# Kernel tuning notes

Hardware: AMD Instinct MI355X
Metric: run time of the kernel (lower is better)

The kernel has to match this reference:

```python
import jax, jax.numpy as jnp
import numpy as np

EPS = 1e-5

def conv1x1(x, w):
    # x: [B,C,T,D,H,W], w: [O,C] -> [B,O,T,D,H,W]
    return jnp.einsum('oc,bctdhw->botdhw', w, x)

def conv4d_3(x, w):
    # 3x3x3x3 4D conv, padding=1, stride=1, decomposed as 3 shifted 3D convs.
    # x: [B,C,T,D,H,W], w: [O,C,3,3,3,3]
    B, C, T, D, H, W = x.shape
    O = w.shape[0]
    xp = jnp.pad(x, ((0, 0), (0, 0), (1, 1), (1, 1), (1, 1), (1, 1)))
    out = None
    for k in range(3):  # small fixed loop over first kernel dim
        xk = xp[:, :, k:k + T]                      # [B,C,T,D+2,H+2,W+2]
        xk = xk.transpose(0, 2, 1, 3, 4, 5).reshape(B * T, C, D + 2, H + 2, W + 2)
        ok = jax.lax.conv_general_dilated(
            xk, w[:, :, k], window_strides=(1, 1, 1), padding='VALID',
            dimension_numbers=('NCDHW', 'OIDHW', 'NCDHW'))  # [B*T,O,D,H,W]
        out = ok if out is None else out + ok
    return out.reshape(B, T, O, D, H, W).transpose(0, 2, 1, 3, 4, 5)

def bn4d(x, g, b):
    # BatchNorm over (B, T, D, H, W) per channel (training-mode batch stats).
    axes = (0, 2, 3, 4, 5)
    m = jnp.mean(x, axis=axes, keepdims=True)
    v = jnp.mean(jnp.square(x - m), axis=axes, keepdims=True)
    sh = (1, -1, 1, 1, 1, 1)
    return (x - m) * jax.lax.rsqrt(v + EPS) * g.reshape(sh) + b.reshape(sh)

def setup_inputs() -> dict:
    key = jax.random.key(0)
    ks = jax.random.split(key, 4)
    B, C, T, D, H, W = 2, 256, 8, 16, 16, 16
    planes = 64
    return {
        'x': jax.random.normal(ks[0], (B, C, T, D, H, W), jnp.float32),
        'w1': jax.random.normal(ks[1], (planes, C), jnp.float32) * 0.05,
        'g1': jnp.ones((planes,), jnp.float32),
        'b1': jnp.zeros((planes,), jnp.float32),
        'w2': jax.random.normal(ks[2], (planes, planes, 3, 3, 3, 3), jnp.float32) * 0.05,
        'g2': jnp.ones((planes,), jnp.float32),
        'b2': jnp.zeros((planes,), jnp.float32),
        'w3': jax.random.normal(ks[3], (4 * planes, planes), jnp.float32) * 0.05,
        'g3': jnp.ones((4 * planes,), jnp.float32),
        'b3': jnp.zeros((4 * planes,), jnp.float32),
    }

def reference(x, w1, g1, b1, w2, g2, b2, w3, g3, b3):
    out = jax.nn.relu(bn4d(conv1x1(x, w1), g1, b1))
    out = jax.nn.relu(bn4d(conv4d_3(out, w2), g2, b2))
    out = bn4d(conv1x1(out, w3), g3, b3)
    return jax.nn.relu(out + x)
```

## Files before the change

kernel.cpp:

```cpp
#include <hip/hip_runtime.h>

#define S_TOT 32768

typedef unsigned short ushortT;
typedef __attribute__((ext_vector_type(8))) short short8;
typedef __attribute__((ext_vector_type(4))) float floatx4;

__device__ __forceinline__ ushortT f2bf(float f) {
    unsigned u = __float_as_uint(f);
    u = (u + 0x7fffu + ((u >> 16) & 1u)) >> 16;
    return (ushortT)u;
}
__device__ __forceinline__ float bf2f(ushortT h) {
    return __uint_as_float(((unsigned)h) << 16);
}
__device__ __forceinline__ uint32_t nrm2(uint32_t u, float a, float bs) {
    float lo = fmaxf(fmaf(a, bf2f((ushortT)(u & 0xffffu)), bs), 0.f);
    float hi = fmaxf(fmaf(a, bf2f((ushortT)(u >> 16)), bs), 0.f);
    return (uint32_t)f2bf(lo) | ((uint32_t)f2bf(hi) << 16);
}

#define NSTRIPE 8
#define STRIDE_ST 768

__global__ __launch_bounds__(256) void k_prep_w(const float* __restrict__ w1,
                                                const float* __restrict__ w2,
                                                const float* __restrict__ w3,
                                                ushortT* __restrict__ wb1,
                                                ushortT* __restrict__ wb2,
                                                ushortT* __restrict__ wb3,
                                                float* __restrict__ stats) {
    int idx = blockIdx.x * 256 + threadIdx.x;
    if (idx < 16384) {
        int e = idx;
        int j = e & 7, o = (e >> 3) & 63, q = (e >> 9) & 3, cc = e >> 11;
        int c = cc * 32 + q * 8 + j;
        wb1[e] = f2bf(w1[o * 256 + c]);
    } else if (idx < 16384 + 331776) {
        int e = idx - 16384;
        int j = e & 7, o = (e >> 3) & 63, cb = (e >> 9) & 7, tap = e >> 12;
        int c = cb * 8 + j;
        wb2[e] = f2bf(w2[((size_t)o * 64 + c) * 81 + tap]);
    } else if (idx < 16384 + 331776 + 16384) {
        int e = idx - 348160;
        int j = e & 7, o = (e >> 3) & 255, g = e >> 11;
        int ks = g >> 2, q = g & 3;
        int c = ks * 32 + q * 8 + j;
        wb3[e] = f2bf(w3[o * 64 + c]);
    } else if (idx < 364544 + NSTRIPE * STRIDE_ST) {
        stats[idx - 364544] = 0.f;
    }
}

__global__ __launch_bounds__(256) void k_coef(const float* __restrict__ stats,
                                              int off, int nch,
                                              const float* __restrict__ g,
                                              const float* __restrict__ bb,
                                              float* __restrict__ coef) {
    int c = threadIdx.x;
    if (c >= nch) return;
    float s = 0.f, qv = 0.f;
#pragma unroll
    for (int p = 0; p < NSTRIPE; ++p) {
        s  += stats[p * STRIDE_ST + off + c];
        qv += stats[p * STRIDE_ST + off + nch + c];
    }
    const float inv_n = 1.f / 65536.f;
    float mu = s * inv_n, var = qv * inv_n - mu * mu;
    float a  = g[c] * rsqrtf(var + 1e-5f);
    coef[2 * c]     = a;
    coef[2 * c + 1] = bb[c] - mu * a;
}

__global__ __launch_bounds__(256) void k_conv1_mfma(const float* __restrict__ x,
                                                    const ushortT* __restrict__ wb1,
                                                    ushortT* __restrict__ y1bf,
                                                    float* __restrict__ stats) {
    __shared__ __align__(16) ushortT xb[128 * 40];

    int tid = threadIdx.x;
    int blk = blockIdx.x;
    int b  = blk >> 8;
    int n0 = (blk & 255) * 128;

    int lane = tid & 63;
    int wv   = tid >> 6;
    int m    = lane & 15;
    int q    = lane >> 4;

    int c_loc = tid & 31;
    int ng    = tid >> 5;

    floatx4 acc[8];
#pragma unroll
    for (int i = 0; i < 8; ++i) acc[i] = (floatx4){0.f, 0.f, 0.f, 0.f};

    for (int cc = 0; cc < 8; ++cc) {
        short8 afr = *(const short8*)(wb1 + (((cc * 4 + q) * 64) + wv * 16 + m) * 8);

        __syncthreads();
        {
            int c = cc * 32 + c_loc;
            const float* xp = x + ((size_t)(b * 256 + c)) * S_TOT + n0 + ng * 16;
#pragma unroll
            for (int k = 0; k < 4; ++k) {
                float4 v = *(const float4*)(xp + k * 4);
                int nb = ng * 16 + k * 4;
                xb[(nb + 0) * 40 + c_loc] = f2bf(v.x);
                xb[(nb + 1) * 40 + c_loc] = f2bf(v.y);
                xb[(nb + 2) * 40 + c_loc] = f2bf(v.z);
                xb[(nb + 3) * 40 + c_loc] = f2bf(v.w);
            }
        }
        __syncthreads();

#pragma unroll
        for (int pt = 0; pt < 8; ++pt) {
            short8 bfr = *(const short8*)(xb + (pt * 16 + m) * 40 + q * 8);
            acc[pt] = __builtin_amdgcn_mfma_f32_16x16x32_bf16(afr, bfr, acc[pt], 0, 0, 0);
        }
    }

#pragma unroll
    for (int pt = 0; pt < 8; ++pt) {
#pragma unroll
        for (int r = 0; r < 4; ++r) {
            int o = wv * 16 + q * 4 + r;
            y1bf[((size_t)(b * 64 + o)) * S_TOT + n0 + pt * 16 + m] = f2bf(acc[pt][r]);
        }
    }

    float ssum[4] = {0.f, 0.f, 0.f, 0.f}, ssq[4] = {0.f, 0.f, 0.f, 0.f};
#pragma unroll
    for (int pt = 0; pt < 8; ++pt)
#pragma unroll
        for (int r = 0; r < 4; ++r) {
            float v = acc[pt][r];
            ssum[r] += v;
            ssq[r]  += v * v;
        }
#pragma unroll
    for (int off = 1; off < 16; off <<= 1)
#pragma unroll
        for (int r = 0; r < 4; ++r) {
            ssum[r] += __shfl_xor(ssum[r], off);
            ssq[r]  += __shfl_xor(ssq[r], off);
        }
    if (m == 0) {
        float* st = stats + (blk & (NSTRIPE - 1)) * STRIDE_ST;
#pragma unroll
        for (int r = 0; r < 4; ++r) {
            int o = wv * 16 + q * 4 + r;
            atomicAdd(st + o, ssum[r]);
            atomicAdd(st + 64 + o, ssq[r]);
        }
    }
}

__global__ __launch_bounds__(256, 2) void k_conv2_mfma(
        const ushortT* __restrict__ y1bf,
        const ushortT* __restrict__ wb2,
        const float* __restrict__ coef1,
        float* __restrict__ stats,
        ushortT* __restrict__ y2bf) {
    __shared__ __align__(16) ushortT xs[180 * 64];
    __shared__ float st2[128];

    int tid = threadIdx.x;
    int blk = blockIdx.x;
    int b  = blk >> 8;
    int t  = (blk >> 5) & 7;
    int d  = (blk >> 1) & 15;
    int h0 = (blk & 1) * 8;

    int lane = tid & 63;
    int wv   = tid >> 6;
    int m    = lane & 15;
    int q    = lane >> 4;
    int wp   = wv & 1;
    int wo   = wv >> 1;

    int c2      = tid & 31;
    int prbase  = tid >> 5;

    if (tid < 128) st2[tid] = 0.f;

    int c0 = 2 * c2, c1v = c0 + 1;
    float2 cA = *(const float2*)(coef1 + 2 * c0);
    float2 cB = *(const float2*)(coef1 + 2 * c1v);
    float a0 = cA.x, bb0 = cA.y, a1 = cB.x, bb1 = cB.y;

    floatx4 acc[2][4];
#pragma unroll
    for (int i = 0; i < 2; ++i)
#pragma unroll
        for (int j = 0; j < 4; ++j) acc[i][j] = (floatx4){0.f, 0.f, 0.f, 0.f};

    const size_t cstride = 32768;
    uint32_t* xsd = (uint32_t*)xs;

    for (int ktd = 0; ktd < 9; ++ktd) {
        int kt = ktd / 3, kd = ktd - kt * 3;
        int tt = t + kt - 1;
        int dd = d + kd - 1;
        bool pv = (tt >= 0 && tt < 8 && dd >= 0 && dd < 16);
        if (!pv) continue;

        short8 afr[9][2][2];
#pragma unroll
        for (int khw = 0; khw < 9; ++khw) {
            int tap = ktd * 9 + khw;
#pragma unroll
            for (int ks = 0; ks < 2; ++ks)
#pragma unroll
                for (int ot = 0; ot < 2; ++ot) {
                    afr[khw][ks][ot] = *(const short8*)(wb2 +
                        (((size_t)(tap * 8 + ks * 4 + q)) * 64 + wo * 32 + ot * 16 + m) * 8);
                }
        }

        __syncthreads();

        for (int pr = prbase; pr < 10; pr += 8) {
            int hin = h0 + pr - 1;
            uint32_t pack[18];
            if (hin >= 0 && hin < 16) {
                const ushortT* p0 = y1bf +
                    (((size_t)(b * 64 + c0) * 8 + tt) * 16 + dd) * 256 + hin * 16;
                const ushortT* p1 = p0 + cstride;
                uint4 r0 = *(const uint4*)p0;
                uint4 r1 = *(const uint4*)(p0 + 8);
                uint4 s0v = *(const uint4*)p1;
                uint4 s1v = *(const uint4*)(p1 + 8);
                uint32_t ra[8] = {r0.x, r0.y, r0.z, r0.w, r1.x, r1.y, r1.z, r1.w};
                uint32_t sa[8] = {s0v.x, s0v.y, s0v.z, s0v.w, s1v.x, s1v.y, s1v.z, s1v.w};
#pragma unroll
                for (int k = 0; k < 8; ++k) {
                    ra[k] = nrm2(ra[k], a0, bb0);
                    sa[k] = nrm2(sa[k], a1, bb1);
                }
                pack[0] = 0; pack[17] = 0;
#pragma unroll
                for (int k = 0; k < 8; ++k) {
                    pack[1 + 2 * k] = (ra[k] & 0xffffu) | (sa[k] << 16);
                    pack[2 + 2 * k] = (ra[k] >> 16) | (sa[k] & 0xffff0000u);
                }
            } else {
#pragma unroll
                for (int k = 0; k < 18; ++k) pack[k] = 0;
            }
            int pb = pr * 18;
#pragma unroll
            for (int k = 0; k < 18; ++k) {
                int ppos = pb + k;
                xsd[ppos * 32 + ((((c2 >> 2) ^ (ppos & 7)) << 2) | (c2 & 3))] = pack[k];
            }
        }
        __syncthreads();

#pragma unroll
        for (int kh = 0; kh < 3; ++kh) {
#pragma unroll
            for (int kw = 0; kw < 3; ++kw) {
                int khw = kh * 3 + kw;
#pragma unroll
                for (int nt = 0; nt < 4; ++nt) {
                    int ppos = (wp * 4 + nt + kh) * 18 + m + kw;
                    int sw = (ppos & 7);
                    const ushortT* row = xs + ppos * 64;
                    short8 b0 = *(const short8*)(row + (((0 * 4 + q) ^ sw) << 3));
                    short8 b1f = *(const short8*)(row + (((1 * 4 + q) ^ sw) << 3));
                    acc[0][nt] = __builtin_amdgcn_mfma_f32_16x16x32_bf16(
                        afr[khw][0][0], b0, acc[0][nt], 0, 0, 0);
                    acc[1][nt] = __builtin_amdgcn_mfma_f32_16x16x32_bf16(
                        afr[khw][0][1], b0, acc[1][nt], 0, 0, 0);
                    acc[0][nt] = __builtin_amdgcn_mfma_f32_16x16x32_bf16(
                        afr[khw][1][0], b1f, acc[0][nt], 0, 0, 0);
                    acc[1][nt] = __builtin_amdgcn_mfma_f32_16x16x32_bf16(
                        afr[khw][1][1], b1f, acc[1][nt], 0, 0, 0);
                }
            }
        }
    }

#pragma unroll
    for (int ot = 0; ot < 2; ++ot) {
#pragma unroll
        for (int nt = 0; nt < 4; ++nt) {
#pragma unroll
            for (int r = 0; r < 4; ++r) {
                int o  = wo * 32 + ot * 16 + q * 4 + r;
                int hh = h0 + wp * 4 + nt;
                y2bf[(((size_t)(b * 64 + o) * 8 + t) * 16 + d) * 256 + hh * 16 + m] =
                    f2bf(acc[ot][nt][r]);
            }
        }
    }

    float ss[2][4], sqv[2][4];
#pragma unroll
    for (int ot = 0; ot < 2; ++ot)
#pragma unroll
        for (int r = 0; r < 4; ++r) {
            float s = 0.f, qv = 0.f;
#pragma unroll
            for (int nt = 0; nt < 4; ++nt) {
                float v = acc[ot][nt][r];
                s += v; qv += v * v;
            }
            ss[ot][r] = s; sqv[ot][r] = qv;
        }
#pragma unroll
    for (int off = 1; off < 16; off <<= 1)
#pragma unroll
        for (int ot = 0; ot < 2; ++ot)
#pragma unroll
            for (int r = 0; r < 4; ++r) {
                ss[ot][r]  += __shfl_xor(ss[ot][r], off);
                sqv[ot][r] += __shfl_xor(sqv[ot][r], off);
            }
    if (m == 0) {
#pragma unroll
        for (int ot = 0; ot < 2; ++ot)
#pragma unroll
            for (int r = 0; r < 4; ++r) {
                int o = wo * 32 + ot * 16 + q * 4 + r;
                atomicAdd(&st2[o], ss[ot][r]);
                atomicAdd(&st2[64 + o], sqv[ot][r]);
            }
    }
    __syncthreads();
    if (tid < 128)
        atomicAdd(stats + (blk & (NSTRIPE - 1)) * STRIDE_ST + 128 + tid, st2[tid]);
}

__global__ __launch_bounds__(256) void k_conv3_mfma(const ushortT* __restrict__ y2bf,
                                                    const ushortT* __restrict__ wb3,
                                                    const float* __restrict__ coef2,
                                                    float* __restrict__ stats,
                                                    float* __restrict__ y3) {
    __shared__ __align__(16) ushortT yb[64 * 72];

    int tid = threadIdx.x;
    int blk = blockIdx.x;
    int b  = blk >> 9;
    int n0 = (blk & 511) * 64;

    int lane = tid & 63;
    int wv   = tid >> 6;
    int m    = lane & 15;
    int q    = lane >> 4;

    for (int idx = tid; idx < 512; idx += 256) {
        int c = idx >> 3, k = idx & 7;
        float2 cc2 = *(const float2*)(coef2 + 2 * c);
        float a = cc2.x, bs = cc2.y;
        uint4 v = *(const uint4*)(y2bf + ((size_t)(b * 64 + c)) * S_TOT + n0 + k * 8);
        uint32_t va[4] = {v.x, v.y, v.z, v.w};
#pragma unroll
        for (int p = 0; p < 4; ++p) {
            float lo = fmaxf(fmaf(a, bf2f((ushortT)(va[p] & 0xffffu)), bs), 0.f);
            float hi = fmaxf(fmaf(a, bf2f((ushortT)(va[p] >> 16)), bs), 0.f);
            yb[(k * 8 + 2 * p)     * 72 + c] = f2bf(lo);
            yb[(k * 8 + 2 * p + 1) * 72 + c] = f2bf(hi);
        }
    }
    __syncthreads();

    floatx4 acc[4][4];
#pragma unroll
    for (int i = 0; i < 4; ++i)
#pragma unroll
        for (int j = 0; j < 4; ++j) acc[i][j] = (floatx4){0.f, 0.f, 0.f, 0.f};

#pragma unroll
    for (int ks = 0; ks < 2; ++ks) {
        short8 afr[4];
#pragma unroll
        for (int ot = 0; ot < 4; ++ot)
            afr[ot] = *(const short8*)(wb3 +
                (((ks * 4 + q) * 256) + wv * 64 + ot * 16 + m) * 8);
#pragma unroll
        for (int pt = 0; pt < 4; ++pt) {
            short8 bfr = *(const short8*)(yb + (pt * 16 + m) * 72 + ks * 32 + q * 8);
#pragma unroll
            for (int ot = 0; ot < 4; ++ot)
                acc[ot][pt] = __builtin_amdgcn_mfma_f32_16x16x32_bf16(
                    afr[ot], bfr, acc[ot][pt], 0, 0, 0);
        }
    }

#pragma unroll
    for (int ot = 0; ot < 4; ++ot) {
#pragma unroll
        for (int pt = 0; pt < 4; ++pt) {
#pragma unroll
            for (int r = 0; r < 4; ++r) {
                int o = wv * 64 + ot * 16 + q * 4 + r;
                y3[((size_t)(b * 256 + o)) * S_TOT + n0 + pt * 16 + m] = acc[ot][pt][r];
            }
        }
    }

    float ssum[4][4], ssq[4][4];
#pragma unroll
    for (int ot = 0; ot < 4; ++ot)
#pragma unroll
        for (int r = 0; r < 4; ++r) {
            float s = 0.f, qv = 0.f;
#pragma unroll
            for (int pt = 0; pt < 4; ++pt) {
                float v = acc[ot][pt][r];
                s += v; qv += v * v;
            }
            ssum[ot][r] = s; ssq[ot][r] = qv;
        }
#pragma unroll
    for (int off = 1; off < 16; off <<= 1)
#pragma unroll
        for (int ot = 0; ot < 4; ++ot)
#pragma unroll
            for (int r = 0; r < 4; ++r) {
                ssum[ot][r] += __shfl_xor(ssum[ot][r], off);
                ssq[ot][r]  += __shfl_xor(ssq[ot][r], off);
            }
    if (m == 0) {
        float* st = stats + (blk & (NSTRIPE - 1)) * STRIDE_ST;
#pragma unroll
        for (int ot = 0; ot < 4; ++ot)
#pragma unroll
            for (int r = 0; r < 4; ++r) {
                int o = wv * 64 + ot * 16 + q * 4 + r;
                atomicAdd(st + 256 + o, ssum[ot][r]);
                atomicAdd(st + 512 + o, ssq[ot][r]);
            }
    }
}

__global__ __launch_bounds__(256) void k_final(const float* __restrict__ x,
                                               const float* __restrict__ stats,
                                               const float* __restrict__ g,
                                               const float* __restrict__ bb,
                                               float* __restrict__ out) {
    size_t i = ((size_t)blockIdx.x * 256 + threadIdx.x) * 4;
    int o = (int)((blockIdx.x >> 5) & 255);
    float s = 0.f, qv = 0.f;
#pragma unroll
    for (int p = 0; p < NSTRIPE; ++p) {
        s  += stats[p * STRIDE_ST + 256 + o];
        qv += stats[p * STRIDE_ST + 512 + o];
    }
    const float n = 65536.f;
    float mean = s / n;
    float var  = qv / n - mean * mean;
    float a  = g[o] * rsqrtf(var + 1e-5f);
    float bs = bb[o] - mean * a;
    float4 y  = *(float4*)(out + i);
    float4 xv = *(const float4*)(x + i);
    float4 r;
    r.x = fmaxf(a * y.x + bs + xv.x, 0.f);
    r.y = fmaxf(a * y.y + bs + xv.y, 0.f);
    r.z = fmaxf(a * y.z + bs + xv.z, 0.f);
    r.w = fmaxf(a * y.w + bs + xv.w, 0.f);
    *(float4*)(out + i) = r;
}

extern "C" void kernel_launch(void* const* d_in, const int* in_sizes, int n_in,
                              void* d_out, int out_size, void* d_ws, size_t ws_size,
                              hipStream_t stream) {
    const float* x  = (const float*)d_in[0];
    const float* w1 = (const float*)d_in[1];
    const float* g1 = (const float*)d_in[2];
    const float* b1 = (const float*)d_in[3];
    const float* w2 = (const float*)d_in[4];
    const float* g2 = (const float*)d_in[5];
    const float* b2 = (const float*)d_in[6];
    const float* w3 = (const float*)d_in[7];
    const float* g3 = (const float*)d_in[8];
    const float* b3 = (const float*)d_in[9];

    char* ws = (char*)d_ws;
    ushortT* y1bf = (ushortT*)(ws);
    ushortT* y2bf = (ushortT*)(ws + 8388608);
    ushortT* wb1  = (ushortT*)(ws + 16777216);
    ushortT* wb2  = (ushortT*)(ws + 16809984);
    ushortT* wb3  = (ushortT*)(ws + 17473536);
    float*   stats = (float*)(ws + 17506304);
    float*   coef1 = (float*)(ws + 17530880);
    float*   coef2 = (float*)(ws + 17531392);
    float* y3 = (float*)d_out;

    k_prep_w     <<<1448,  256, 0, stream>>>(w1, w2, w3, wb1, wb2, wb3, stats);
    k_conv1_mfma <<<512,   256, 0, stream>>>(x, wb1, y1bf, stats);
    k_coef       <<<1,     256, 0, stream>>>(stats, 0, 64, g1, b1, coef1);
    k_conv2_mfma <<<512,   256, 0, stream>>>(y1bf, wb2, coef1, stats, y2bf);
    k_coef       <<<1,     256, 0, stream>>>(stats, 128, 64, g2, b2, coef2);
    k_conv3_mfma <<<1024,  256, 0, stream>>>(y2bf, wb3, coef2, stats, y3);
    k_final      <<<16384, 256, 0, stream>>>(x, stats, g3, b3, y3);
}
```

Measured before the change: 268.5 us.

## Pre-normalize conv1 output in separate pass and halve conv2 spatial tile

Adds a separate elementwise kernel that applies BN1 scale/shift and ReLU to the conv1 output once, writing a normalized bf16 copy. The conv2 kernel then loads that copy directly instead of re-normalizing every halo row for each of the 9 (t,d) taps. Conv2 now covers 4 h-rows per block instead of 8, which doubles the grid, shrinks the shared tile, and raises the occupancy hint to 4. In exchange there is an extra launch, an extra 8 MB read and write to a new workspace buffer, and a larger halo overhead (6 loaded rows per 4 output rows instead of 10 per 8).

```diff
diff --git a/kernel.cpp b/kernel.cpp
--- a/kernel.cpp
+++ b/kernel.cpp
@@ -72,6 +72,21 @@
     coef[2 * c + 1] = bb[c] - mu * a;
 }
 
+__global__ __launch_bounds__(256) void k_prep(const ushortT* __restrict__ yin,
+                                              const float* __restrict__ coef,
+                                              ushortT* __restrict__ yout) {
+    size_t i = ((size_t)blockIdx.x * 256 + threadIdx.x) * 8;
+    int c = (int)((i >> 15) & 63);
+    float2 cf = *(const float2*)(coef + 2 * c);
+    uint4 v = *(const uint4*)(yin + i);
+    uint4 r;
+    r.x = nrm2(v.x, cf.x, cf.y);
+    r.y = nrm2(v.y, cf.x, cf.y);
+    r.z = nrm2(v.z, cf.x, cf.y);
+    r.w = nrm2(v.w, cf.x, cf.y);
+    *(uint4*)(yout + i) = r;
+}
+
 __global__ __launch_bounds__(256) void k_conv1_mfma(const float* __restrict__ x,
                                                     const ushortT* __restrict__ wb1,
                                                     ushortT* __restrict__ y1bf,
@@ -157,21 +172,20 @@
     }
 }
 
-__global__ __launch_bounds__(256, 2) void k_conv2_mfma(
-        const ushortT* __restrict__ y1bf,
+__global__ __launch_bounds__(256, 4) void k_conv2_mfma(
+        const ushortT* __restrict__ y1n,
         const ushortT* __restrict__ wb2,
-        const float* __restrict__ coef1,
         float* __restrict__ stats,
         ushortT* __restrict__ y2bf) {
-    __shared__ __align__(16) ushortT xs[180 * 64];
+    __shared__ __align__(16) ushortT xs[108 * 64];
     __shared__ float st2[128];
 
     int tid = threadIdx.x;
     int blk = blockIdx.x;
-    int b  = blk >> 8;
-    int t  = (blk >> 5) & 7;
-    int d  = (blk >> 1) & 15;
-    int h0 = (blk & 1) * 8;
+    int b  = blk >> 9;
+    int t  = (blk >> 6) & 7;
+    int d  = (blk >> 2) & 15;
+    int h0 = (blk & 3) * 4;
 
     int lane = tid & 63;
     int wv   = tid >> 6;
@@ -185,16 +199,11 @@
 
     if (tid < 128) st2[tid] = 0.f;
 
-    int c0 = 2 * c2, c1v = c0 + 1;
-    float2 cA = *(const float2*)(coef1 + 2 * c0);
-    float2 cB = *(const float2*)(coef1 + 2 * c1v);
-    float a0 = cA.x, bb0 = cA.y, a1 = cB.x, bb1 = cB.y;
-
-    floatx4 acc[2][4];
+    floatx4 acc[2][2];
 #pragma unroll
     for (int i = 0; i < 2; ++i)
 #pragma unroll
-        for (int j = 0; j < 4; ++j) acc[i][j] = (floatx4){0.f, 0.f, 0.f, 0.f};
+        for (int j = 0; j < 2; ++j) acc[i][j] = (floatx4){0.f, 0.f, 0.f, 0.f};
 
     const size_t cstride = 32768;
     uint32_t* xsd = (uint32_t*)xs;
@@ -221,12 +230,12 @@
 
         __syncthreads();
 
-        for (int pr = prbase; pr < 10; pr += 8) {
-            int hin = h0 + pr - 1;
+        if (prbase < 6) {
+            int hin = h0 + prbase - 1;
             uint32_t pack[18];
             if (hin >= 0 && hin < 16) {
-                const ushortT* p0 = y1bf +
-                    (((size_t)(b * 64 + c0) * 8 + tt) * 16 + dd) * 256 + hin * 16;
+                const ushortT* p0 = y1n +
+                    (((size_t)(b * 64 + 2 * c2) * 8 + tt) * 16 + dd) * 256 + hin * 16;
                 const ushortT* p1 = p0 + cstride;
                 uint4 r0 = *(const uint4*)p0;
                 uint4 r1 = *(const uint4*)(p0 + 8);
@@ -234,11 +243,6 @@
                 uint4 s1v = *(const uint4*)(p1 + 8);
                 uint32_t ra[8] = {r0.x, r0.y, r0.z, r0.w, r1.x, r1.y, r1.z, r1.w};
                 uint32_t sa[8] = {s0v.x, s0v.y, s0v.z, s0v.w, s1v.x, s1v.y, s1v.z, s1v.w};
-#pragma unroll
-                for (int k = 0; k < 8; ++k) {
-                    ra[k] = nrm2(ra[k], a0, bb0);
-                    sa[k] = nrm2(sa[k], a1, bb1);
-                }
                 pack[0] = 0; pack[17] = 0;
 #pragma unroll
                 for (int k = 0; k < 8; ++k) {
@@ -249,7 +253,7 @@
 #pragma unroll
                 for (int k = 0; k < 18; ++k) pack[k] = 0;
             }
-            int pb = pr * 18;
+            int pb = prbase * 18;
 #pragma unroll
             for (int k = 0; k < 18; ++k) {
                 int ppos = pb + k;
@@ -264,11 +268,11 @@
             for (int kw = 0; kw < 3; ++kw) {
                 int khw = kh * 3 + kw;
 #pragma unroll
-                for (int nt = 0; nt < 4; ++nt) {
-                    int ppos = (wp * 4 + nt + kh) * 18 + m + kw;
+                for (int nt = 0; nt < 2; ++nt) {
+                    int ppos = (wp * 2 + nt + kh) * 18 + m + kw;
                     int sw = (ppos & 7);
                     const ushortT* row = xs + ppos * 64;
-                    short8 b0 = *(const short8*)(row + (((0 * 4 + q) ^ sw) << 3));
+                    short8 b0  = *(const short8*)(row + (((0 * 4 + q) ^ sw) << 3));
                     short8 b1f = *(const short8*)(row + (((1 * 4 + q) ^ sw) << 3));
                     acc[0][nt] = __builtin_amdgcn_mfma_f32_16x16x32_bf16(
                         afr[khw][0][0], b0, acc[0][nt], 0, 0, 0);
@@ -286,11 +290,11 @@
 #pragma unroll
     for (int ot = 0; ot < 2; ++ot) {
 #pragma unroll
-        for (int nt = 0; nt < 4; ++nt) {
+        for (int nt = 0; nt < 2; ++nt) {
 #pragma unroll
             for (int r = 0; r < 4; ++r) {
                 int o  = wo * 32 + ot * 16 + q * 4 + r;
-                int hh = h0 + wp * 4 + nt;
+                int hh = h0 + wp * 2 + nt;
                 y2bf[(((size_t)(b * 64 + o) * 8 + t) * 16 + d) * 256 + hh * 16 + m] =
                     f2bf(acc[ot][nt][r]);
             }
@@ -304,7 +308,7 @@
         for (int r = 0; r < 4; ++r) {
             float s = 0.f, qv = 0.f;
 #pragma unroll
-            for (int nt = 0; nt < 4; ++nt) {
+            for (int nt = 0; nt < 2; ++nt) {
                 float v = acc[ot][nt][r];
                 s += v; qv += v * v;
             }
@@ -481,19 +485,21 @@
 
     char* ws = (char*)d_ws;
     ushortT* y1bf = (ushortT*)(ws);
-    ushortT* y2bf = (ushortT*)(ws + 8388608);
-    ushortT* wb1  = (ushortT*)(ws + 16777216);
-    ushortT* wb2  = (ushortT*)(ws + 16809984);
-    ushortT* wb3  = (ushortT*)(ws + 17473536);
-    float*   stats = (float*)(ws + 17506304);
-    float*   coef1 = (float*)(ws + 17530880);
-    float*   coef2 = (float*)(ws + 17531392);
+    ushortT* y1n  = (ushortT*)(ws + 8388608);
+    ushortT* y2bf = (ushortT*)(ws + 16777216);
+    ushortT* wb1  = (ushortT*)(ws + 25165824);
+    ushortT* wb2  = (ushortT*)(ws + 25198592);
+    ushortT* wb3  = (ushortT*)(ws + 25862144);
+    float*   stats = (float*)(ws + 25894912);
+    float*   coef1 = (float*)(ws + 25919488);
+    float*   coef2 = (float*)(ws + 25920000);
     float* y3 = (float*)d_out;
 
     k_prep_w     <<<1448,  256, 0, stream>>>(w1, w2, w3, wb1, wb2, wb3, stats);
     k_conv1_mfma <<<512,   256, 0, stream>>>(x, wb1, y1bf, stats);
     k_coef       <<<1,     256, 0, stream>>>(stats, 0, 64, g1, b1, coef1);
-    k_conv2_mfma <<<512,   256, 0, stream>>>(y1bf, wb2, coef1, stats, y2bf);
+    k_prep       <<<2048,  256, 0, stream>>>(y1bf, coef1, y1n);
+    k_conv2_mfma <<<1024,  256, 0, stream>>>(y1n, wb2, stats, y2bf);
     k_coef       <<<1,     256, 0, stream>>>(stats, 128, 64, g2, b2, coef2);
     k_conv3_mfma <<<1024,  256, 0, stream>>>(y2bf, wb3, coef2, stats, y3);
     k_final      <<<16384, 256, 0, stream>>>(x, stats, g3, b3, y3);
```

Result: slower. 526.3 us (+96.1%).
